# Kernel tuning notes

Measured on AMD Instinct MI355X. Metric: run time of the kernel, lower is better.

Reference implementation:

```python
import jax, jax.numpy as jnp
import numpy as np

N = 50000
E = 800000
GENE = 256
H = 128
BN_EPS = 1e-5


def _lin(key, fan_in, fan_out):
    k1, k2 = jax.random.split(key)
    w = jax.random.normal(k1, (fan_in, fan_out), jnp.float32) * (1.0 / np.sqrt(fan_in))
    b = jax.random.normal(k2, (fan_out,), jnp.float32) * 0.01
    return w, b


def setup_inputs() -> dict:
    key = jax.random.key(0)
    ks = jax.random.split(key, 32)
    inp = {}
    inp['x'] = jax.random.normal(ks[0], (N, GENE), jnp.float32)
    inp['edge_index'] = jax.random.randint(ks[1], (2, E), 0, N, jnp.int32)
    dims = [(GENE, H), (H, 2 * H), (2 * H, H), (H, H // 2)]
    ki = 2
    for i, (din, dout) in enumerate(dims, start=1):
        wa, ba = _lin(ks[ki], din, dout); ki += 1
        wb, bb = _lin(ks[ki], dout, dout); ki += 1
        inp[f'w{i}a'], inp[f'b{i}a'] = wa, ba
        inp[f'w{i}b'], inp[f'b{i}b'] = wb, bb
        inp[f'bn{i}_g'] = jnp.ones((dout,), jnp.float32)
        inp[f'bn{i}_b'] = jnp.zeros((dout,), jnp.float32)
        inp[f'bn{i}_m'] = jax.random.normal(ks[ki], (dout,), jnp.float32) * 0.1; ki += 1
        inp[f'bn{i}_v'] = jax.random.uniform(ks[ki], (dout,), jnp.float32, 0.5, 1.5); ki += 1
    wc, bc = _lin(ks[ki], H // 2, 2)
    inp['wc'], inp['bc'] = wc, bc
    return inp


def _gin_layer(h, src, dst, wa, ba, wb, bb, g, be, m, v):
    # GINConv (eps=0): z = x + sum_{j in N(i)} x_j, then 2-layer MLP
    agg = jax.ops.segment_sum(h[src], dst, num_segments=N)
    z = h + agg
    z = jax.nn.relu(z @ wa + ba) @ wb + bb
    # BatchNorm1d (eval: running stats) + ReLU
    z = (z - m) * jax.lax.rsqrt(v + BN_EPS) * g + be
    return jax.nn.relu(z)


def reference(x, edge_index,
              w1a, b1a, w1b, b1b, bn1_g, bn1_b, bn1_m, bn1_v,
              w2a, b2a, w2b, b2b, bn2_g, bn2_b, bn2_m, bn2_v,
              w3a, b3a, w3b, b3b, bn3_g, bn3_b, bn3_m, bn3_v,
              w4a, b4a, w4b, b4b, bn4_g, bn4_b, bn4_m, bn4_v,
              wc, bc):
    src, dst = edge_index[0], edge_index[1]
    h = _gin_layer(x, src, dst, w1a, b1a, w1b, b1b, bn1_g, bn1_b, bn1_m, bn1_v)
    h = _gin_layer(h, src, dst, w2a, b2a, w2b, b2b, bn2_g, bn2_b, bn2_m, bn2_v)
    h = _gin_layer(h, src, dst, w3a, b3a, w3b, b3b, bn3_g, bn3_b, bn3_m, bn3_v)
    h = _gin_layer(h, src, dst, w4a, b4a, w4b, b4b, bn4_g, bn4_b, bn4_m, bn4_v)
    return h @ wc + bc
```

## Files before the change

kernel.cpp:

```cpp
#include <hip/hip_runtime.h>

#define N_NODES 50000
#define N_EDGES 800000
#define BN_EPS 1e-5f
#define K_BUCK 196
#define PART_B 256
#define CHUNK 3125

typedef __attribute__((ext_vector_type(8))) short bshort8;
typedef __attribute__((ext_vector_type(4))) float f32x4;

__device__ inline float bf2f(unsigned int u16) {
    return __uint_as_float(u16 << 16);
}
__device__ inline unsigned short f2bf(float f) {
    unsigned int u = __float_as_uint(f);
    u = (u + 0x7FFFu + ((u >> 16) & 1u)) >> 16;
    return (unsigned short)u;
}


__device__ inline int block_exscan256(int v, int tid, int* total) {
    int lane = tid & 63;
    int wave = tid >> 6;
    int incl = v;
#pragma unroll
    for (int off = 1; off < 64; off <<= 1) {
        int t = __shfl_up(incl, off, 64);
        if (lane >= off) incl += t;
    }
    __shared__ int wsum[4];
    if (lane == 63) wsum[wave] = incl;
    __syncthreads();
    int w0 = wsum[0], w1 = wsum[1], w2 = wsum[2], w3 = wsum[3];
    __syncthreads();
    int wofs = (wave > 0 ? w0 : 0) + (wave > 1 ? w1 : 0) + (wave > 2 ? w2 : 0);
    *total = w0 + w1 + w2 + w3;
    return wofs + incl - v;
}

__global__ __launch_bounds__(256) void scan_reduce_kernel(const int* __restrict__ in,
                                                          int* __restrict__ bsum, int n) {
    int tid = threadIdx.x;
    int i = blockIdx.x * 256 + tid;
    int v = (i < n) ? in[i] : 0;
    int lane = tid & 63;
    int wave = tid >> 6;
#pragma unroll
    for (int off = 32; off > 0; off >>= 1) v += __shfl_down(v, off, 64);
    __shared__ int wsum[4];
    if (lane == 0) wsum[wave] = v;
    __syncthreads();
    if (tid == 0) bsum[blockIdx.x] = wsum[0] + wsum[1] + wsum[2] + wsum[3];
}

__global__ __launch_bounds__(256) void scan_bsum_kernel(int* __restrict__ bsum, int B) {
    int tid = threadIdx.x;
    int v = (tid < B) ? bsum[tid] : 0;
    int total;
    int excl = block_exscan256(v, tid, &total);
    if (tid < B) bsum[tid] = excl;
}

__global__ __launch_bounds__(256) void scan_apply_kernel(const int* __restrict__ in,
                                                         const int* __restrict__ bsum,
                                                         int* __restrict__ out, int n) {
    int tid = threadIdx.x;
    int i = blockIdx.x * 256 + tid;
    int v = (i < n) ? in[i] : 0;
    int total;
    int excl = block_exscan256(v, tid, &total);
    if (i < n) out[i] = bsum[blockIdx.x] + excl;
}


__global__ __launch_bounds__(256) void bucket_count_kernel(const int* __restrict__ dst,
                                                           int* __restrict__ deg,
                                                           int* __restrict__ cnt) {
    __shared__ int lcnt[K_BUCK];
    int tid = threadIdx.x;
    for (int i = tid; i < K_BUCK; i += 256) lcnt[i] = 0;
    __syncthreads();
    int start = blockIdx.x * CHUNK;
    for (int it = tid; it < CHUNK; it += 256) {
        int d = dst[start + it];
        atomicAdd(&lcnt[d >> 8], 1);
        atomicAdd(&deg[d], 1);
    }
    __syncthreads();
    for (int i = tid; i < K_BUCK; i += 256) cnt[i * PART_B + blockIdx.x] = lcnt[i];
}

__global__ __launch_bounds__(256) void partition_kernel(const int* __restrict__ src,
                                                        const int* __restrict__ dst,
                                                        const int* __restrict__ base,
                                                        uint2* __restrict__ P) {
    __shared__ int lofs[K_BUCK];
    int tid = threadIdx.x;
    for (int i = tid; i < K_BUCK; i += 256) lofs[i] = base[i * PART_B + blockIdx.x];
    __syncthreads();
    int start = blockIdx.x * CHUNK;
    for (int it = tid; it < CHUNK; it += 256) {
        int e = start + it;
        int d = dst[e], s = src[e];
        int p = atomicAdd(&lofs[d >> 8], 1);
        P[p] = make_uint2((unsigned)d, (unsigned)s);
    }
}

__global__ __launch_bounds__(256) void fine_scatter_kernel(const uint2* __restrict__ P,
                                                           const int* __restrict__ base,
                                                           const int* __restrict__ deg,
                                                           int* __restrict__ rowptr,
                                                           int* __restrict__ col) {
    __shared__ int wloc[256];
    int b = blockIdx.x;
    int tid = threadIdx.x;
    int nbase = b << 8;
    int nn = min(256, N_NODES - nbase);
    int d = (tid < nn) ? deg[nbase + tid] : 0;
    int total;
    int excl = block_exscan256(d, tid, &total);
    int start = base[b * PART_B];
    int rp = start + excl;
    if (tid < nn) {
        rowptr[nbase + tid] = rp;
        wloc[tid] = rp;
    }
    if (b == K_BUCK - 1 && tid == 0) rowptr[N_NODES] = N_EDGES;
    __syncthreads();
    int end = (b + 1 < K_BUCK) ? base[(b + 1) * PART_B] : N_EDGES;
    for (int e = start + tid; e < end; e += 256) {
        uint2 pr = P[e];
        int rank = atomicAdd(&wloc[pr.x - nbase], 1);
        col[rank] = (int)pr.y;
    }
}


struct WT8 {
    const float* src[8];
    unsigned short* dst[8];
    int K[8];
    int N[8];
};

__global__ __launch_bounds__(256) void wtconv_kernel(WT8 p) {
    int wi = blockIdx.y;
    int K = p.K[wi], N = p.N[wi];
    int idx = blockIdx.x * 256 + threadIdx.x;
    if (idx >= K * N) return;
    int logn = 31 - __clz(N);
    int n = idx & (N - 1);
    int k = idx >> logn;
    p.dst[wi][(size_t)n * K + k] = f2bf(p.src[wi][idx]);
}

__global__ __launch_bounds__(256) void wpconv_kernel(WT8 p) {
    int wi = blockIdx.y;
    int K = p.K[wi], N = p.N[wi];
    int idx = blockIdx.x * 256 + threadIdx.x;
    if (idx >= K * N) return;
    int S = K >> 5;
    int logs = 31 - __clz(S);
    int j = idx & 7;
    int l = (idx >> 3) & 63;
    int rest = idx >> 9;
    int s = rest & (S - 1);
    int t = rest >> logs;
    int k = s * 32 + ((l >> 4) << 3) + j;
    int n = t * 16 + (l & 15);
    p.dst[wi][idx] = f2bf(p.src[wi][(size_t)k * N + n]);
}


__device__ inline void acc8(uint4 v, float* a) {
    a[0] += bf2f(v.x & 0xFFFFu); a[1] += __uint_as_float(v.x & 0xFFFF0000u);
    a[2] += bf2f(v.y & 0xFFFFu); a[3] += __uint_as_float(v.y & 0xFFFF0000u);
    a[4] += bf2f(v.z & 0xFFFFu); a[5] += __uint_as_float(v.z & 0xFFFF0000u);
    a[6] += bf2f(v.w & 0xFFFFu); a[7] += __uint_as_float(v.w & 0xFFFF0000u);
}

template <int LPN, bool RELU>
__global__ __launch_bounds__(256) void aggregate_bf16_kernel(
    const unsigned short* __restrict__ h, const int* __restrict__ rowptr,
    const int* __restrict__ col, const float* __restrict__ bias,
    unsigned short* __restrict__ z, int n) {
    const int gpb = 256 / LPN;
    int gid = threadIdx.x / LPN;
    int l = threadIdx.x % LPN;
    int node = blockIdx.x * gpb + gid;
    if (node >= n) return;
    const uint4* hv = (const uint4*)h;
    float a[8] = {};
    uint4 vs = hv[(size_t)node * LPN + l];
    int s = rowptr[node], epos = rowptr[node + 1];
    int e = s;
    for (; e + 4 <= epos; e += 4) {
        int j0 = col[e], j1 = col[e + 1], j2 = col[e + 2], j3 = col[e + 3];
        uint4 v0 = hv[(size_t)j0 * LPN + l];
        uint4 v1 = hv[(size_t)j1 * LPN + l];
        uint4 v2 = hv[(size_t)j2 * LPN + l];
        uint4 v3 = hv[(size_t)j3 * LPN + l];
        acc8(v0, a); acc8(v1, a); acc8(v2, a); acc8(v3, a);
    }
    if (e + 1 < epos) {
        int j0 = col[e], j1 = col[e + 1];
        uint4 v0 = hv[(size_t)j0 * LPN + l];
        uint4 v1 = hv[(size_t)j1 * LPN + l];
        acc8(v0, a); acc8(v1, a);
        e += 2;
    }
    if (e < epos) {
        acc8(hv[(size_t)col[e] * LPN + l], a);
    }
    acc8(vs, a);
    if (RELU) {
        float4 b0 = *(const float4*)(bias + l * 8);
        float4 b1 = *(const float4*)(bias + l * 8 + 4);
        a[0] = fmaxf(a[0] + b0.x, 0.f); a[1] = fmaxf(a[1] + b0.y, 0.f);
        a[2] = fmaxf(a[2] + b0.z, 0.f); a[3] = fmaxf(a[3] + b0.w, 0.f);
        a[4] = fmaxf(a[4] + b1.x, 0.f); a[5] = fmaxf(a[5] + b1.y, 0.f);
        a[6] = fmaxf(a[6] + b1.z, 0.f); a[7] = fmaxf(a[7] + b1.w, 0.f);
    }
    uint4 o;
    o.x = (unsigned int)f2bf(a[0]) | ((unsigned int)f2bf(a[1]) << 16);
    o.y = (unsigned int)f2bf(a[2]) | ((unsigned int)f2bf(a[3]) << 16);
    o.z = (unsigned int)f2bf(a[4]) | ((unsigned int)f2bf(a[5]) << 16);
    o.w = (unsigned int)f2bf(a[6]) | ((unsigned int)f2bf(a[7]) << 16);
    ((uint4*)z)[(size_t)node * LPN + l] = o;
}


__device__ inline void epi_coeff(int mode, int c, const float* bias, const float* g,
                                 const float* be, const float* mu, const float* var,
                                 float* s, float* sh) {
    *s = 1.f; *sh = 0.f;
    if (mode == 0) {
        *sh = bias[c];
    } else if (mode == 1) {
        float t = g[c] * rsqrtf(var[c] + BN_EPS);
        *s = t;
        *sh = be[c] - mu[c] * t + bias[c] * t;
    }
}


template <int NT, bool F32A, bool CLS>
__global__ __launch_bounds__(256) void mfma_gemm2_kernel(
    const void* __restrict__ Ain, const unsigned short* __restrict__ Wt,
    const float* __restrict__ bias, unsigned short* __restrict__ C,
    int M, int K, int Nn, int mode, int gxblocks, int gy,
    const float* __restrict__ g, const float* __restrict__ be,
    const float* __restrict__ mu, const float* __restrict__ var,
    const float* __restrict__ wcls, const float* __restrict__ bcls,
    float* __restrict__ outp) {
    constexpr int BM = 128, BK = 64;
    constexpr int BN = NT * 16;
    constexpr int LDA = BK + 8;
    constexpr int LDB = BK + 8;
    constexpr int LDE = BN + 8;
    constexpr int NB_LD = (BN * BK / 8) / 256;
    __shared__ __align__(16) unsigned short smem[BM * LDA + BN * LDB];
    unsigned short* As = smem;
    unsigned short* Bs = smem + BM * LDA;
    unsigned short* Ep = smem;

    int id = blockIdx.x;
    int lo = id & 7;
    int t = id >> 3;
    int y = t % gy;
    int x = ((t / gy) << 3) | lo;
    if (x >= gxblocks) return;

    const int tid = threadIdx.x;
    const int wv = tid >> 6;
    const int ln = tid & 63;
    const int l15 = ln & 15;
    const int quad = ln >> 4;
    const int row0 = x * BM;
    const int col0 = y * BN;

    const unsigned short* A16 = (const unsigned short*)Ain;
    const float* A32 = (const float*)Ain;

    uint4 Ar[4], Br[NB_LD];

    auto loadA = [&](int k0) {
#pragma unroll
        for (int u = 0; u < 4; ++u) {
            int idx2 = tid + 256 * u;
            int r = idx2 >> 3, cg = (idx2 & 7) * 8;
            int gr = row0 + r;
            if (gr >= M) gr = M - 1;
            if (F32A) {
                float4 f0 = *(const float4*)(A32 + (size_t)gr * K + k0 + cg);
                float4 f1 = *(const float4*)(A32 + (size_t)gr * K + k0 + cg + 4);
                uint4 o;
                o.x = (unsigned)f2bf(f0.x) | ((unsigned)f2bf(f0.y) << 16);
                o.y = (unsigned)f2bf(f0.z) | ((unsigned)f2bf(f0.w) << 16);
                o.z = (unsigned)f2bf(f1.x) | ((unsigned)f2bf(f1.y) << 16);
                o.w = (unsigned)f2bf(f1.z) | ((unsigned)f2bf(f1.w) << 16);
                Ar[u] = o;
            } else {
                Ar[u] = *(const uint4*)(A16 + (size_t)gr * K + k0 + cg);
            }
        }
    };
    auto loadB = [&](int k0) {
#pragma unroll
        for (int u = 0; u < NB_LD; ++u) {
            int idx2 = tid + 256 * u;
            int r = idx2 >> 3, cg = (idx2 & 7) * 8;
            Br[u] = *(const uint4*)(Wt + (size_t)(col0 + r) * K + k0 + cg);
        }
    };
    auto stage = [&]() {
#pragma unroll
        for (int u = 0; u < 4; ++u) {
            int idx2 = tid + 256 * u;
            int r = idx2 >> 3, cg = (idx2 & 7) * 8;
            *(uint4*)(&As[r * LDA + cg]) = Ar[u];
        }
#pragma unroll
        for (int u = 0; u < NB_LD; ++u) {
            int idx2 = tid + 256 * u;
            int r = idx2 >> 3, cg = (idx2 & 7) * 8;
            *(uint4*)(&Bs[r * LDB + cg]) = Br[u];
        }
    };

    f32x4 acc[2][NT] = {};
    const int KT = K >> 6;
    loadA(0);
    loadB(0);
    for (int kt = 0; kt < KT; ++kt) {
        if (kt > 0) __syncthreads();
        stage();
        __syncthreads();
        if (kt + 1 < KT) {
            loadA((kt + 1) * 64);
            loadB((kt + 1) * 64);
        }
#pragma unroll
        for (int kh = 0; kh < 2; ++kh) {
            bshort8 af[2];
#pragma unroll
            for (int mt = 0; mt < 2; ++mt)
                af[mt] = *(const bshort8*)(&As[(wv * 32 + mt * 16 + l15) * LDA + kh * 32 + quad * 8]);
#pragma unroll
            for (int nt = 0; nt < NT; ++nt) {
                bshort8 bf = *(const bshort8*)(&Bs[(nt * 16 + l15) * LDB + kh * 32 + quad * 8]);
                acc[0][nt] = __builtin_amdgcn_mfma_f32_16x16x32_bf16(af[0], bf, acc[0][nt], 0, 0, 0);
                acc[1][nt] = __builtin_amdgcn_mfma_f32_16x16x32_bf16(af[1], bf, acc[1][nt], 0, 0, 0);
            }
        }
    }

    __syncthreads();
#pragma unroll
    for (int nt = 0; nt < NT; ++nt) {
        int c = col0 + nt * 16 + l15;
        float s, sh;
        epi_coeff(mode, c, bias, g, be, mu, var, &s, &sh);
#pragma unroll
        for (int mt = 0; mt < 2; ++mt) {
            int rl = wv * 32 + mt * 16 + quad * 4;
#pragma unroll
            for (int r = 0; r < 4; ++r) {
                float v = acc[mt][nt][r] * s + sh;
                if (mode != 2) v = fmaxf(v, 0.f);
                Ep[(rl + r) * LDE + nt * 16 + l15] = f2bf(v);
            }
        }
    }
    __syncthreads();
    if (CLS) {
        int r = tid >> 1, j = tid & 1;
        int grow = row0 + r;
        if (grow < M) {
            float s = 0.f;
#pragma unroll 8
            for (int k = 0; k < 64; ++k)
                s += bf2f(Ep[r * LDE + k]) * wcls[k * 2 + j];
            outp[(size_t)grow * 2 + j] = s + bcls[j];
        }
    } else {
        constexpr int CGR = BN / 8;
        constexpr int NU = BM * CGR / 256;
#pragma unroll
        for (int u = 0; u < NU; ++u) {
            int idx2 = tid + 256 * u;
            int r = idx2 / CGR, cg = (idx2 % CGR) * 8;
            int grow = row0 + r;
            if (grow < M)
                *(uint4*)(C + (size_t)grow * Nn + col0 + cg) = *(const uint4*)(&Ep[r * LDE + cg]);
        }
    }
}


template <int KIN, int DH>
__global__ __launch_bounds__(256, 4) void packed_gemm_kernel(
    const unsigned short* __restrict__ A, const unsigned short* __restrict__ Wp,
    int mode, const float* __restrict__ bias, const float* __restrict__ g,
    const float* __restrict__ be, const float* __restrict__ mu, const float* __restrict__ var,
    unsigned short* __restrict__ C, int M) {
    constexpr int BM = 64, BK = 64;
    constexpr int LDA = BK + 8;
    constexpr int LDE = DH + 8;
    constexpr int NT = DH / 64;
    constexpr int KT = KIN / 64;
    constexpr int S = KIN / 32;
    __shared__ __align__(16) unsigned short smem[BM * LDE];
    unsigned short* As = smem;
    unsigned short* Ep = smem;

    const int tid = threadIdx.x;
    const int wv = tid >> 6;
    const int ln = tid & 63;
    const int l15 = ln & 15;
    const int quad = ln >> 4;
    const int tb = wv * NT;
    const int ch = wv * (DH / 4);
    const int row0 = blockIdx.x * BM;

    uint4 Ar[2];
    auto loadA = [&](int k0) {
#pragma unroll
        for (int u = 0; u < 2; ++u) {
            int idx2 = tid + 256 * u;
            int r = idx2 >> 3, cg = (idx2 & 7) * 8;
            int gr = row0 + r;
            if (gr >= M) gr = M - 1;
            Ar[u] = *(const uint4*)(A + (size_t)gr * KIN + k0 + cg);
        }
    };
    auto stageA = [&]() {
#pragma unroll
        for (int u = 0; u < 2; ++u) {
            int idx2 = tid + 256 * u;
            int r = idx2 >> 3, cg = (idx2 & 7) * 8;
            *(uint4*)(&As[r * LDA + cg]) = Ar[u];
        }
    };
    auto loadB = [&](int s, bshort8* d) {
#pragma unroll
        for (int nt = 0; nt < NT; ++nt)
            d[nt] = *(const bshort8*)(Wp + ((size_t)((tb + nt) * S + s) * 64 + ln) * 8);
    };

    f32x4 acc[4][NT] = {};
    bshort8 bf[NT], bnx[NT];
    loadA(0);
    loadB(0, bf);
    for (int kt = 0; kt < KT; ++kt) {
        if (kt > 0) __syncthreads();
        stageA();
        __syncthreads();
        if (kt + 1 < KT) loadA((kt + 1) * 64);
#pragma unroll
        for (int kh = 0; kh < 2; ++kh) {
            int st = kt * 2 + kh;
            if (st + 1 < S) loadB(st + 1, bnx);
            bshort8 af[4];
#pragma unroll
            for (int mt = 0; mt < 4; ++mt)
                af[mt] = *(const bshort8*)(&As[(mt * 16 + l15) * LDA + kh * 32 + quad * 8]);
#pragma unroll
            for (int nt = 0; nt < NT; ++nt)
#pragma unroll
                for (int mt = 0; mt < 4; ++mt)
                    acc[mt][nt] = __builtin_amdgcn_mfma_f32_16x16x32_bf16(af[mt], bf[nt], acc[mt][nt], 0, 0, 0);
            if (st + 1 < S) {
#pragma unroll
                for (int nt = 0; nt < NT; ++nt) bf[nt] = bnx[nt];
            }
        }
    }
    __syncthreads();
#pragma unroll
    for (int nt = 0; nt < NT; ++nt) {
        int c = ch + nt * 16 + l15;
        float s, sh;
        epi_coeff(mode, c, bias, g, be, mu, var, &s, &sh);
#pragma unroll
        for (int mt = 0; mt < 4; ++mt) {
            int rl = mt * 16 + quad * 4;
#pragma unroll
            for (int r = 0; r < 4; ++r) {
                float v = acc[mt][nt][r] * s + sh;
                if (mode != 2) v = fmaxf(v, 0.f);
                Ep[(rl + r) * LDE + c] = f2bf(v);
            }
        }
    }
    __syncthreads();
    constexpr int CGR = DH / 8;
    constexpr int NU = BM * CGR / 256;
#pragma unroll
    for (int u = 0; u < NU; ++u) {
        int idx2 = tid + 256 * u;
        int r = idx2 / CGR, cg = (idx2 % CGR) * 8;
        int grow = row0 + r;
        if (grow < M)
            *(uint4*)(C + (size_t)grow * DH + cg) = *(const uint4*)(&Ep[r * LDE + cg]);
    }
}


template <int KIN, int DH1, int DH2>
__global__ __launch_bounds__(256, 3) void fused_mlp_kernel(
    const unsigned short* __restrict__ A,
    const unsigned short* __restrict__ Wp1, const unsigned short* __restrict__ Wp2,
    int mode1, const float* __restrict__ b1, const float* __restrict__ g1,
    const float* __restrict__ be1, const float* __restrict__ mu1, const float* __restrict__ var1,
    int mode2, const float* __restrict__ b2, const float* __restrict__ g2,
    const float* __restrict__ be2, const float* __restrict__ mu2, const float* __restrict__ var2,
    unsigned short* __restrict__ C, int M) {
    constexpr int BM = 64, BK = 64;
    constexpr int LDA = BK + 8;
    constexpr int LT1 = DH1 + 8;
    constexpr int LDE = DH2 + 8;
    constexpr int NT1 = DH1 / 64;
    constexpr int NT2 = DH2 / 64;
    constexpr int KT = KIN / 64;
    constexpr int S1 = KIN / 32;
    constexpr int S2 = DH1 / 32;
    __shared__ __align__(16) unsigned short smem[BM * LT1];
    unsigned short* As = smem;
    unsigned short* T1 = smem;

    const int tid = threadIdx.x;
    const int wv = tid >> 6;
    const int ln = tid & 63;
    const int l15 = ln & 15;
    const int quad = ln >> 4;
    const int tb1 = wv * NT1;
    const int tb2 = wv * NT2;
    const int ch1 = wv * (DH1 / 4);
    const int ch2 = wv * (DH2 / 4);
    const int row0 = blockIdx.x * BM;

    uint4 Ar[2];
    auto loadA = [&](int k0) {
#pragma unroll
        for (int u = 0; u < 2; ++u) {
            int idx2 = tid + 256 * u;
            int r = idx2 >> 3, cg = (idx2 & 7) * 8;
            int gr = row0 + r;
            if (gr >= M) gr = M - 1;
            Ar[u] = *(const uint4*)(A + (size_t)gr * KIN + k0 + cg);
        }
    };
    auto stageA = [&]() {
#pragma unroll
        for (int u = 0; u < 2; ++u) {
            int idx2 = tid + 256 * u;
            int r = idx2 >> 3, cg = (idx2 & 7) * 8;
            *(uint4*)(&As[r * LDA + cg]) = Ar[u];
        }
    };
    auto loadB1 = [&](int s, bshort8* d) {
#pragma unroll
        for (int nt = 0; nt < NT1; ++nt)
            d[nt] = *(const bshort8*)(Wp1 + ((size_t)((tb1 + nt) * S1 + s) * 64 + ln) * 8);
    };
    auto loadB2 = [&](int s, bshort8* d) {
#pragma unroll
        for (int nt = 0; nt < NT2; ++nt)
            d[nt] = *(const bshort8*)(Wp2 + ((size_t)((tb2 + nt) * S2 + s) * 64 + ln) * 8);
    };

    f32x4 acc1[4][NT1] = {};
    bshort8 bf[NT1], bnx[NT1], bf2[NT2];
    loadA(0);
    loadB1(0, bf);
    loadB2(0, bf2);
    for (int kt = 0; kt < KT; ++kt) {
        if (kt > 0) __syncthreads();
        stageA();
        __syncthreads();
        if (kt + 1 < KT) loadA((kt + 1) * 64);
#pragma unroll
        for (int kh = 0; kh < 2; ++kh) {
            int st = kt * 2 + kh;
            if (st + 1 < S1) loadB1(st + 1, bnx);
            bshort8 af[4];
#pragma unroll
            for (int mt = 0; mt < 4; ++mt)
                af[mt] = *(const bshort8*)(&As[(mt * 16 + l15) * LDA + kh * 32 + quad * 8]);
#pragma unroll
            for (int nt = 0; nt < NT1; ++nt)
#pragma unroll
                for (int mt = 0; mt < 4; ++mt)
                    acc1[mt][nt] = __builtin_amdgcn_mfma_f32_16x16x32_bf16(af[mt], bf[nt], acc1[mt][nt], 0, 0, 0);
            if (st + 1 < S1) {
#pragma unroll
                for (int nt = 0; nt < NT1; ++nt) bf[nt] = bnx[nt];
            }
        }
    }
    __syncthreads();
#pragma unroll
    for (int nt = 0; nt < NT1; ++nt) {
        int c = ch1 + nt * 16 + l15;
        float s, sh;
        epi_coeff(mode1, c, b1, g1, be1, mu1, var1, &s, &sh);
#pragma unroll
        for (int mt = 0; mt < 4; ++mt) {
            int rl = mt * 16 + quad * 4;
#pragma unroll
            for (int r = 0; r < 4; ++r) {
                float v = acc1[mt][nt][r] * s + sh;
                if (mode1 != 2) v = fmaxf(v, 0.f);
                T1[(rl + r) * LT1 + c] = f2bf(v);
            }
        }
    }
    __syncthreads();

    f32x4 acc2[4][NT2] = {};
    bshort8 bnx2[NT2];
#pragma unroll
    for (int ks = 0; ks < S2; ++ks) {
        if (ks + 1 < S2) loadB2(ks + 1, bnx2);
        bshort8 af[4];
#pragma unroll
        for (int mt = 0; mt < 4; ++mt)
            af[mt] = *(const bshort8*)(&T1[(mt * 16 + l15) * LT1 + ks * 32 + quad * 8]);
#pragma unroll
        for (int nt = 0; nt < NT2; ++nt)
#pragma unroll
            for (int mt = 0; mt < 4; ++mt)
                acc2[mt][nt] = __builtin_amdgcn_mfma_f32_16x16x32_bf16(af[mt], bf2[nt], acc2[mt][nt], 0, 0, 0);
        if (ks + 1 < S2) {
#pragma unroll
            for (int nt = 0; nt < NT2; ++nt) bf2[nt] = bnx2[nt];
        }
    }
    __syncthreads();

    unsigned short* Ep = T1;
#pragma unroll
    for (int nt = 0; nt < NT2; ++nt) {
        int c = ch2 + nt * 16 + l15;
        float s, sh;
        epi_coeff(mode2, c, b2, g2, be2, mu2, var2, &s, &sh);
#pragma unroll
        for (int mt = 0; mt < 4; ++mt) {
            int rl = mt * 16 + quad * 4;
#pragma unroll
            for (int r = 0; r < 4; ++r) {
                float v = acc2[mt][nt][r] * s + sh;
                if (mode2 != 2) v = fmaxf(v, 0.f);
                Ep[(rl + r) * LDE + c] = f2bf(v);
            }
        }
    }
    __syncthreads();
    constexpr int CGR = DH2 / 8;
    constexpr int NU = BM * CGR / 256;
#pragma unroll
    for (int u = 0; u < NU; ++u) {
        int idx2 = tid + 256 * u;
        int r = idx2 / CGR, cg = (idx2 % CGR) * 8;
        int grow = row0 + r;
        if (grow < M)
            *(uint4*)(C + (size_t)grow * DH2 + cg) = *(const uint4*)(&Ep[r * LDE + cg]);
    }
}


extern "C" void kernel_launch(void* const* d_in, const int* in_sizes, int n_in,
                              void* d_out, int out_size, void* d_ws, size_t ws_size,
                              hipStream_t stream) {
    const float* x = (const float*)d_in[0];
    const int* ei = (const int*)d_in[1];
    const int* src = ei;
    const int* dst = ei + N_EDGES;
    const float* w[4][2];
    const float* b[4][2];
    const float* bng[4];
    const float* bnb[4];
    const float* bnm[4];
    const float* bnv[4];
    int idx = 2;
    for (int i = 0; i < 4; ++i) {
        w[i][0] = (const float*)d_in[idx++];
        b[i][0] = (const float*)d_in[idx++];
        w[i][1] = (const float*)d_in[idx++];
        b[i][1] = (const float*)d_in[idx++];
        bng[i] = (const float*)d_in[idx++];
        bnb[i] = (const float*)d_in[idx++];
        bnm[i] = (const float*)d_in[idx++];
        bnv[i] = (const float*)d_in[idx++];
    }
    const float* wc = (const float*)d_in[idx++];
    const float* bc = (const float*)d_in[idx++];
    float* out = (float*)d_out;

    char* ws = (char*)d_ws;
    size_t off = 0;
    auto alloc = [&](size_t bytes) {
        char* p = ws + off;
        off = (off + bytes + 255) & ~(size_t)255;
        return p;
    };
    int* deg = (int*)alloc((size_t)N_NODES * 4);
    int* rowptr = (int*)alloc((size_t)(N_NODES + 1) * 4);
    int* cnt = (int*)alloc((size_t)K_BUCK * PART_B * 4);
    int* bsum2 = (int*)alloc((size_t)K_BUCK * 4);
    int* col = (int*)alloc((size_t)N_EDGES * 4);
    uint2* P = (uint2*)alloc((size_t)N_EDGES * 8);
    unsigned short* bufA = (unsigned short*)alloc((size_t)N_NODES * 256 * 2);
    unsigned short* bufB = (unsigned short*)alloc((size_t)N_NODES * 256 * 2);
    unsigned short* bufC = (unsigned short*)alloc((size_t)N_NODES * 256 * 2);
    const int dims_in[4] = {256, 128, 256, 128};
    const int dims_h[4] = {128, 256, 128, 64};
    unsigned short* wt[4][2];
    unsigned short* wp[4][2];
    for (int L = 0; L < 4; ++L) {
        wt[L][0] = (unsigned short*)alloc((size_t)dims_in[L] * dims_h[L] * 2);
        wt[L][1] = (unsigned short*)alloc((size_t)dims_h[L] * dims_h[L] * 2);
        wp[L][0] = (unsigned short*)alloc((size_t)dims_in[L] * dims_h[L] * 2);
        wp[L][1] = (unsigned short*)alloc((size_t)dims_h[L] * dims_h[L] * 2);
    }
    (void)ws_size;

    WT8 p;
    for (int L = 0; L < 4; ++L) {
        p.src[L * 2] = w[L][0];     p.dst[L * 2] = wt[L][0];
        p.K[L * 2] = dims_in[L];    p.N[L * 2] = dims_h[L];
        p.src[L * 2 + 1] = w[L][1]; p.dst[L * 2 + 1] = wt[L][1];
        p.K[L * 2 + 1] = dims_h[L]; p.N[L * 2 + 1] = dims_h[L];
    }
    wtconv_kernel<<<dim3(256, 8), 256, 0, stream>>>(p);
    WT8 q = p;
    for (int L = 0; L < 4; ++L) {
        q.dst[L * 2] = wp[L][0];
        q.dst[L * 2 + 1] = wp[L][1];
    }
    wpconv_kernel<<<dim3(256, 8), 256, 0, stream>>>(q);

    hipMemsetAsync(deg, 0, (size_t)N_NODES * 4, stream);
    bucket_count_kernel<<<PART_B, 256, 0, stream>>>(dst, deg, cnt);
    scan_reduce_kernel<<<K_BUCK, 256, 0, stream>>>(cnt, bsum2, K_BUCK * PART_B);
    scan_bsum_kernel<<<1, 256, 0, stream>>>(bsum2, K_BUCK);
    scan_apply_kernel<<<K_BUCK, 256, 0, stream>>>(cnt, bsum2, cnt, K_BUCK * PART_B);
    partition_kernel<<<PART_B, 256, 0, stream>>>(src, dst, cnt, P);
    fine_scatter_kernel<<<K_BUCK, 256, 0, stream>>>(P, cnt, deg, rowptr, col);

    const int gx = (N_NODES + 127) / 128;
    const int gxp = ((gx + 7) / 8) * 8;
    const int gx64 = (N_NODES + 63) / 64;
    const int M = N_NODES;

    mfma_gemm2_kernel<8, true, false><<<gxp, 256, 0, stream>>>(
        x, wt[0][0], nullptr, bufA, M, 256, 128, 2, gx, 1,
        nullptr, nullptr, nullptr, nullptr, nullptr, nullptr, nullptr);
    aggregate_bf16_kernel<16, true><<<(N_NODES + 15) / 16, 256, 0, stream>>>(
        bufA, rowptr, col, b[0][0], bufB, N_NODES);
    packed_gemm_kernel<128, 128><<<gx64, 256, 0, stream>>>(
        bufB, wp[0][1], 1, b[0][1], bng[0], bnb[0], bnm[0], bnv[0], bufC, M);

    aggregate_bf16_kernel<16, false><<<(N_NODES + 15) / 16, 256, 0, stream>>>(
        bufC, rowptr, col, nullptr, bufA, N_NODES);
    fused_mlp_kernel<128, 256, 256><<<gx64, 256, 0, stream>>>(
        bufA, wp[1][0], wp[1][1],
        0, b[1][0], nullptr, nullptr, nullptr, nullptr,
        1, b[1][1], bng[1], bnb[1], bnm[1], bnv[1],
        bufC, M);

    packed_gemm_kernel<256, 128><<<gx64, 256, 0, stream>>>(
        bufC, wp[2][0], 2, nullptr, nullptr, nullptr, nullptr, nullptr, bufA, M);
    aggregate_bf16_kernel<16, true><<<(N_NODES + 15) / 16, 256, 0, stream>>>(
        bufA, rowptr, col, b[2][0], bufB, N_NODES);

    fused_mlp_kernel<128, 128, 64><<<gx64, 256, 0, stream>>>(
        bufB, wp[2][1], wp[3][0],
        1, b[2][1], bng[2], bnb[2], bnm[2], bnv[2],
        2, nullptr, nullptr, nullptr, nullptr, nullptr,
        bufA, M);

    aggregate_bf16_kernel<8, true><<<(N_NODES + 31) / 32, 256, 0, stream>>>(
        bufA, rowptr, col, b[3][0], bufB, N_NODES);
    mfma_gemm2_kernel<4, false, true><<<gxp, 256, 0, stream>>>(
        bufB, wt[3][1], b[3][1], nullptr, M, 64, 64, 1, gx, 1,
        bng[3], bnb[3], bnm[3], bnv[3], wc, bc, out);
}
```

Before: 419.6 us.

## Fuse neighbor aggregation into following GEMM/MLP kernels via shared-memory head

```diff
diff --git a/kernel.cpp b/kernel.cpp
--- a/kernel.cpp
+++ b/kernel.cpp
@@ -181,54 +181,62 @@
     a[6] += bf2f(v.w & 0xFFFFu); a[7] += __uint_as_float(v.w & 0xFFFF0000u);
 }
 
-template <int LPN, bool RELU>
-__global__ __launch_bounds__(256) void aggregate_bf16_kernel(
-    const unsigned short* __restrict__ h, const int* __restrict__ rowptr,
-    const int* __restrict__ col, const float* __restrict__ bias,
-    unsigned short* __restrict__ z, int n) {
-    const int gpb = 256 / LPN;
-    int gid = threadIdx.x / LPN;
-    int l = threadIdx.x % LPN;
-    int node = blockIdx.x * gpb + gid;
-    if (node >= n) return;
+template <int KIN, bool RELU>
+__device__ inline void agg_head(const unsigned short* __restrict__ h,
+                                const int* __restrict__ rowptr,
+                                const int* __restrict__ col,
+                                const float* __restrict__ bias,
+                                unsigned short* __restrict__ As,
+                                int row0, int M, int tid) {
+    constexpr int LPN = KIN / 8;
+    constexpr int GPS = 256 / LPN;
+    constexpr int NSW = 64 / GPS;
+    constexpr int LDA = KIN + 8;
     const uint4* hv = (const uint4*)h;
-    float a[8] = {};
-    uint4 vs = hv[(size_t)node * LPN + l];
-    int s = rowptr[node], epos = rowptr[node + 1];
-    int e = s;
-    for (; e + 4 <= epos; e += 4) {
-        int j0 = col[e], j1 = col[e + 1], j2 = col[e + 2], j3 = col[e + 3];
-        uint4 v0 = hv[(size_t)j0 * LPN + l];
-        uint4 v1 = hv[(size_t)j1 * LPN + l];
-        uint4 v2 = hv[(size_t)j2 * LPN + l];
-        uint4 v3 = hv[(size_t)j3 * LPN + l];
-        acc8(v0, a); acc8(v1, a); acc8(v2, a); acc8(v3, a);
-    }
-    if (e + 1 < epos) {
-        int j0 = col[e], j1 = col[e + 1];
-        uint4 v0 = hv[(size_t)j0 * LPN + l];
-        uint4 v1 = hv[(size_t)j1 * LPN + l];
-        acc8(v0, a); acc8(v1, a);
-        e += 2;
-    }
-    if (e < epos) {
-        acc8(hv[(size_t)col[e] * LPN + l], a);
-    }
-    acc8(vs, a);
-    if (RELU) {
-        float4 b0 = *(const float4*)(bias + l * 8);
-        float4 b1 = *(const float4*)(bias + l * 8 + 4);
-        a[0] = fmaxf(a[0] + b0.x, 0.f); a[1] = fmaxf(a[1] + b0.y, 0.f);
-        a[2] = fmaxf(a[2] + b0.z, 0.f); a[3] = fmaxf(a[3] + b0.w, 0.f);
-        a[4] = fmaxf(a[4] + b1.x, 0.f); a[5] = fmaxf(a[5] + b1.y, 0.f);
-        a[6] = fmaxf(a[6] + b1.z, 0.f); a[7] = fmaxf(a[7] + b1.w, 0.f);
-    }
-    uint4 o;
-    o.x = (unsigned int)f2bf(a[0]) | ((unsigned int)f2bf(a[1]) << 16);
-    o.y = (unsigned int)f2bf(a[2]) | ((unsigned int)f2bf(a[3]) << 16);
-    o.z = (unsigned int)f2bf(a[4]) | ((unsigned int)f2bf(a[5]) << 16);
-    o.w = (unsigned int)f2bf(a[6]) | ((unsigned int)f2bf(a[7]) << 16);
-    ((uint4*)z)[(size_t)node * LPN + l] = o;
+    const int l = tid & (LPN - 1);
+    const int g = tid / LPN;
+#pragma unroll
+    for (int sw = 0; sw < NSW; ++sw) {
+        int r = sw * GPS + g;
+        int node = row0 + r;
+        uint4 o = make_uint4(0u, 0u, 0u, 0u);
+        if (node < M) {
+            float a[8] = {};
+            uint4 vs = hv[(size_t)node * LPN + l];
+            int s = rowptr[node], epos = rowptr[node + 1];
+            int e = s;
+            for (; e + 4 <= epos; e += 4) {
+                int j0 = col[e], j1 = col[e + 1], j2 = col[e + 2], j3 = col[e + 3];
+                uint4 v0 = hv[(size_t)j0 * LPN + l];
+                uint4 v1 = hv[(size_t)j1 * LPN + l];
+                uint4 v2 = hv[(size_t)j2 * LPN + l];
+                uint4 v3 = hv[(size_t)j3 * LPN + l];
+                acc8(v0, a); acc8(v1, a); acc8(v2, a); acc8(v3, a);
+            }
+            if (e + 1 < epos) {
+                int j0 = col[e], j1 = col[e + 1];
+                uint4 v0 = hv[(size_t)j0 * LPN + l];
+                uint4 v1 = hv[(size_t)j1 * LPN + l];
+                acc8(v0, a); acc8(v1, a);
+                e += 2;
+            }
+            if (e < epos) acc8(hv[(size_t)col[e] * LPN + l], a);
+            acc8(vs, a);
+            if (RELU) {
+                float4 b0 = *(const float4*)(bias + l * 8);
+                float4 b1 = *(const float4*)(bias + l * 8 + 4);
+                a[0] = fmaxf(a[0] + b0.x, 0.f); a[1] = fmaxf(a[1] + b0.y, 0.f);
+                a[2] = fmaxf(a[2] + b0.z, 0.f); a[3] = fmaxf(a[3] + b0.w, 0.f);
+                a[4] = fmaxf(a[4] + b1.x, 0.f); a[5] = fmaxf(a[5] + b1.y, 0.f);
+                a[6] = fmaxf(a[6] + b1.z, 0.f); a[7] = fmaxf(a[7] + b1.w, 0.f);
+            }
+            o.x = (unsigned int)f2bf(a[0]) | ((unsigned int)f2bf(a[1]) << 16);
+            o.y = (unsigned int)f2bf(a[2]) | ((unsigned int)f2bf(a[3]) << 16);
+            o.z = (unsigned int)f2bf(a[4]) | ((unsigned int)f2bf(a[5]) << 16);
+            o.w = (unsigned int)f2bf(a[6]) | ((unsigned int)f2bf(a[7]) << 16);
+        }
+        *(uint4*)(&As[r * LDA + l * 8]) = o;
+    }
 }
 
 
@@ -246,15 +254,11 @@
 }
 
 
-template <int NT, bool F32A, bool CLS>
+template <int NT, bool F32A>
 __global__ __launch_bounds__(256) void mfma_gemm2_kernel(
     const void* __restrict__ Ain, const unsigned short* __restrict__ Wt,
-    const float* __restrict__ bias, unsigned short* __restrict__ C,
-    int M, int K, int Nn, int mode, int gxblocks, int gy,
-    const float* __restrict__ g, const float* __restrict__ be,
-    const float* __restrict__ mu, const float* __restrict__ var,
-    const float* __restrict__ wcls, const float* __restrict__ bcls,
-    float* __restrict__ outp) {
+    unsigned short* __restrict__ C,
+    int M, int K, int Nn, int mode, int gxblocks, int gy) {
     constexpr int BM = 128, BK = 64;
     constexpr int BN = NT * 16;
     constexpr int LDA = BK + 8;
@@ -360,42 +364,27 @@
     __syncthreads();
 #pragma unroll
     for (int nt = 0; nt < NT; ++nt) {
-        int c = col0 + nt * 16 + l15;
-        float s, sh;
-        epi_coeff(mode, c, bias, g, be, mu, var, &s, &sh);
 #pragma unroll
         for (int mt = 0; mt < 2; ++mt) {
             int rl = wv * 32 + mt * 16 + quad * 4;
 #pragma unroll
             for (int r = 0; r < 4; ++r) {
-                float v = acc[mt][nt][r] * s + sh;
+                float v = acc[mt][nt][r];
                 if (mode != 2) v = fmaxf(v, 0.f);
                 Ep[(rl + r) * LDE + nt * 16 + l15] = f2bf(v);
             }
         }
     }
     __syncthreads();
-    if (CLS) {
-        int r = tid >> 1, j = tid & 1;
+    constexpr int CGR = BN / 8;
+    constexpr int NU = BM * CGR / 256;
+#pragma unroll
+    for (int u = 0; u < NU; ++u) {
+        int idx2 = tid + 256 * u;
+        int r = idx2 / CGR, cg = (idx2 % CGR) * 8;
         int grow = row0 + r;
-        if (grow < M) {
-            float s = 0.f;
-#pragma unroll 8
-            for (int k = 0; k < 64; ++k)
-                s += bf2f(Ep[r * LDE + k]) * wcls[k * 2 + j];
-            outp[(size_t)grow * 2 + j] = s + bcls[j];
-        }
-    } else {
-        constexpr int CGR = BN / 8;
-        constexpr int NU = BM * CGR / 256;
-#pragma unroll
-        for (int u = 0; u < NU; ++u) {
-            int idx2 = tid + 256 * u;
-            int r = idx2 / CGR, cg = (idx2 % CGR) * 8;
-            int grow = row0 + r;
-            if (grow < M)
-                *(uint4*)(C + (size_t)grow * Nn + col0 + cg) = *(const uint4*)(&Ep[r * LDE + cg]);
-        }
+        if (grow < M)
+            *(uint4*)(C + (size_t)grow * Nn + col0 + cg) = *(const uint4*)(&Ep[r * LDE + cg]);
     }
 }
 
@@ -509,25 +498,114 @@
 }
 
 
-template <int KIN, int DH1, int DH2>
-__global__ __launch_bounds__(256, 3) void fused_mlp_kernel(
-    const unsigned short* __restrict__ A,
+template <int KIN, int DH, bool ARELU>
+__global__ __launch_bounds__(256, 4) void agg_gemm_kernel(
+    const unsigned short* __restrict__ h, const int* __restrict__ rowptr,
+    const int* __restrict__ col, const float* __restrict__ abias,
+    const unsigned short* __restrict__ Wp,
+    int mode, const float* __restrict__ bias, const float* __restrict__ g,
+    const float* __restrict__ be, const float* __restrict__ mu, const float* __restrict__ var,
+    unsigned short* __restrict__ C, int M) {
+    constexpr int BM = 64;
+    constexpr int LDA = KIN + 8;
+    constexpr int LDE = DH + 8;
+    constexpr int NT = DH / 64;
+    constexpr int S = KIN / 32;
+    constexpr int LMX = (LDA > LDE) ? LDA : LDE;
+    __shared__ __align__(16) unsigned short smem[BM * LMX];
+    unsigned short* As = smem;
+    unsigned short* Ep = smem;
+
+    const int tid = threadIdx.x;
+    const int wv = tid >> 6;
+    const int ln = tid & 63;
+    const int l15 = ln & 15;
+    const int quad = ln >> 4;
+    const int tb = wv * NT;
+    const int ch = wv * (DH / 4);
+    const int row0 = blockIdx.x * BM;
+
+    auto loadB = [&](int s, bshort8* d) {
+#pragma unroll
+        for (int nt = 0; nt < NT; ++nt)
+            d[nt] = *(const bshort8*)(Wp + ((size_t)((tb + nt) * S + s) * 64 + ln) * 8);
+    };
+
+    bshort8 bf[NT], bnx[NT];
+    loadB(0, bf);
+    agg_head<KIN, ARELU>(h, rowptr, col, abias, As, row0, M, tid);
+    __syncthreads();
+
+    f32x4 acc[4][NT] = {};
+#pragma unroll
+    for (int ks = 0; ks < S; ++ks) {
+        if (ks + 1 < S) loadB(ks + 1, bnx);
+        bshort8 af[4];
+#pragma unroll
+        for (int mt = 0; mt < 4; ++mt)
+            af[mt] = *(const bshort8*)(&As[(mt * 16 + l15) * LDA + (ks >> 1) * 64 + (ks & 1) * 32 + quad * 8]);
+#pragma unroll
+        for (int nt = 0; nt < NT; ++nt)
+#pragma unroll
+            for (int mt = 0; mt < 4; ++mt)
+                acc[mt][nt] = __builtin_amdgcn_mfma_f32_16x16x32_bf16(af[mt], bf[nt], acc[mt][nt], 0, 0, 0);
+        if (ks + 1 < S) {
+#pragma unroll
+            for (int nt = 0; nt < NT; ++nt) bf[nt] = bnx[nt];
+        }
+    }
+    __syncthreads();
+#pragma unroll
+    for (int nt = 0; nt < NT; ++nt) {
+        int c = ch + nt * 16 + l15;
+        float s, sh;
+        epi_coeff(mode, c, bias, g, be, mu, var, &s, &sh);
+#pragma unroll
+        for (int mt = 0; mt < 4; ++mt) {
+            int rl = mt * 16 + quad * 4;
+#pragma unroll
+            for (int r = 0; r < 4; ++r) {
+                float v = acc[mt][nt][r] * s + sh;
+                if (mode != 2) v = fmaxf(v, 0.f);
+                Ep[(rl + r) * LDE + c] = f2bf(v);
+            }
+        }
+    }
+    __syncthreads();
+    constexpr int CGR = DH / 8;
+    constexpr int NU = BM * CGR / 256;
+#pragma unroll
+    for (int u = 0; u < NU; ++u) {
+        int idx2 = tid + 256 * u;
+        int r = idx2 / CGR, cg = (idx2 % CGR) * 8;
+        int grow = row0 + r;
+        if (grow < M)
+            *(uint4*)(C + (size_t)grow * DH + cg) = *(const uint4*)(&Ep[r * LDE + cg]);
+    }
+}
+
+
+template <int KIN, int DH1, int DH2, bool ARELU>
+__global__ __launch_bounds__(256, 3) void agg_mlp_kernel(
+    const unsigned short* __restrict__ h, const int* __restrict__ rowptr,
+    const int* __restrict__ col, const float* __restrict__ abias,
     const unsigned short* __restrict__ Wp1, const unsigned short* __restrict__ Wp2,
     int mode1, const float* __restrict__ b1, const float* __restrict__ g1,
     const float* __restrict__ be1, const float* __restrict__ mu1, const float* __restrict__ var1,
     int mode2, const float* __restrict__ b2, const float* __restrict__ g2,
     const float* __restrict__ be2, const float* __restrict__ mu2, const float* __restrict__ var2,
     unsigned short* __restrict__ C, int M) {
-    constexpr int BM = 64, BK = 64;
-    constexpr int LDA = BK + 8;
+    constexpr int BM = 64;
+    constexpr int LDA = KIN + 8;
     constexpr int LT1 = DH1 + 8;
     constexpr int LDE = DH2 + 8;
     constexpr int NT1 = DH1 / 64;
     constexpr int NT2 = DH2 / 64;
-    constexpr int KT = KIN / 64;
     constexpr int S1 = KIN / 32;
     constexpr int S2 = DH1 / 32;
-    __shared__ __align__(16) unsigned short smem[BM * LT1];
+    constexpr int LM0 = (LDA > LT1) ? LDA : LT1;
+    constexpr int LMX = (LM0 > LDE) ? LM0 : LDE;
+    __shared__ __align__(16) unsigned short smem[BM * LMX];
     unsigned short* As = smem;
     unsigned short* T1 = smem;
 
@@ -542,25 +620,6 @@
     const int ch2 = wv * (DH2 / 4);
     const int row0 = blockIdx.x * BM;
 
-    uint4 Ar[2];
-    auto loadA = [&](int k0) {
-#pragma unroll
-        for (int u = 0; u < 2; ++u) {
-            int idx2 = tid + 256 * u;
-            int r = idx2 >> 3, cg = (idx2 & 7) * 8;
-            int gr = row0 + r;
-            if (gr >= M) gr = M - 1;
-            Ar[u] = *(const uint4*)(A + (size_t)gr * KIN + k0 + cg);
-        }
-    };
-    auto stageA = [&]() {
-#pragma unroll
-        for (int u = 0; u < 2; ++u) {
-            int idx2 = tid + 256 * u;
-            int r = idx2 >> 3, cg = (idx2 & 7) * 8;
-            *(uint4*)(&As[r * LDA + cg]) = Ar[u];
-        }
-    };
     auto loadB1 = [&](int s, bshort8* d) {
 #pragma unroll
         for (int nt = 0; nt < NT1; ++nt)
@@ -572,33 +631,28 @@
             d[nt] = *(const bshort8*)(Wp2 + ((size_t)((tb2 + nt) * S2 + s) * 64 + ln) * 8);
     };
 
-    f32x4 acc1[4][NT1] = {};
     bshort8 bf[NT1], bnx[NT1], bf2[NT2];
-    loadA(0);
     loadB1(0, bf);
     loadB2(0, bf2);
-    for (int kt = 0; kt < KT; ++kt) {
-        if (kt > 0) __syncthreads();
-        stageA();
-        __syncthreads();
-        if (kt + 1 < KT) loadA((kt + 1) * 64);
-#pragma unroll
-        for (int kh = 0; kh < 2; ++kh) {
-            int st = kt * 2 + kh;
-            if (st + 1 < S1) loadB1(st + 1, bnx);
-            bshort8 af[4];
+    agg_head<KIN, ARELU>(h, rowptr, col, abias, As, row0, M, tid);
+    __syncthreads();
+
+    f32x4 acc1[4][NT1] = {};
+#pragma unroll
+    for (int ks = 0; ks < S1; ++ks) {
+        if (ks + 1 < S1) loadB1(ks + 1, bnx);
+        bshort8 af[4];
+#pragma unroll
+        for (int mt = 0; mt < 4; ++mt)
+            af[mt] = *(const bshort8*)(&As[(mt * 16 + l15) * LDA + (ks >> 1) * 64 + (ks & 1) * 32 + quad * 8]);
+#pragma unroll
+        for (int nt = 0; nt < NT1; ++nt)
 #pragma unroll
             for (int mt = 0; mt < 4; ++mt)
-                af[mt] = *(const bshort8*)(&As[(mt * 16 + l15) * LDA + kh * 32 + quad * 8]);
-#pragma unroll
-            for (int nt = 0; nt < NT1; ++nt)
-#pragma unroll
-                for (int mt = 0; mt < 4; ++mt)
-                    acc1[mt][nt] = __builtin_amdgcn_mfma_f32_16x16x32_bf16(af[mt], bf[nt], acc1[mt][nt], 0, 0, 0);
-            if (st + 1 < S1) {
-#pragma unroll
-                for (int nt = 0; nt < NT1; ++nt) bf[nt] = bnx[nt];
-            }
+                acc1[mt][nt] = __builtin_amdgcn_mfma_f32_16x16x32_bf16(af[mt], bf[nt], acc1[mt][nt], 0, 0, 0);
+        if (ks + 1 < S1) {
+#pragma unroll
+            for (int nt = 0; nt < NT1; ++nt) bf[nt] = bnx[nt];
         }
     }
     __syncthreads();
@@ -668,6 +722,84 @@
         int grow = row0 + r;
         if (grow < M)
             *(uint4*)(C + (size_t)grow * DH2 + cg) = *(const uint4*)(&Ep[r * LDE + cg]);
+    }
+}
+
+
+__global__ __launch_bounds__(256, 4) void agg_cls_kernel(
+    const unsigned short* __restrict__ h, const int* __restrict__ rowptr,
+    const int* __restrict__ col, const float* __restrict__ abias,
+    const unsigned short* __restrict__ Wp,
+    const float* __restrict__ bias, const float* __restrict__ g,
+    const float* __restrict__ be, const float* __restrict__ mu, const float* __restrict__ var,
+    const float* __restrict__ wcls, const float* __restrict__ bcls,
+    float* __restrict__ outp, int M) {
+    constexpr int BM = 64, KIN = 64, DH = 64;
+    constexpr int LDA = KIN + 8;
+    constexpr int LDE = DH + 8;
+    constexpr int NT = 1;
+    constexpr int S = KIN / 32;
+    __shared__ __align__(16) unsigned short smem[BM * LDA];
+    unsigned short* As = smem;
+    unsigned short* Ep = smem;
+
+    const int tid = threadIdx.x;
+    const int wv = tid >> 6;
+    const int ln = tid & 63;
+    const int l15 = ln & 15;
+    const int quad = ln >> 4;
+    const int tb = wv;
+    const int ch = wv * 16;
+    const int row0 = blockIdx.x * BM;
+
+    auto loadB = [&](int s, bshort8* d) {
+        d[0] = *(const bshort8*)(Wp + ((size_t)(tb * S + s) * 64 + ln) * 8);
+    };
+
+    bshort8 bf[NT], bnx[NT];
+    loadB(0, bf);
+    agg_head<KIN, true>(h, rowptr, col, abias, As, row0, M, tid);
+    __syncthreads();
+
+    f32x4 acc[4][NT] = {};
+#pragma unroll
+    for (int ks = 0; ks < S; ++ks) {
+        if (ks + 1 < S) loadB(ks + 1, bnx);
+        bshort8 af[4];
+#pragma unroll
+        for (int mt = 0; mt < 4; ++mt)
+            af[mt] = *(const bshort8*)(&As[(mt * 16 + l15) * LDA + ks * 32 + quad * 8]);
+#pragma unroll
+        for (int mt = 0; mt < 4; ++mt)
+            acc[mt][0] = __builtin_amdgcn_mfma_f32_16x16x32_bf16(af[mt], bf[0], acc[mt][0], 0, 0, 0);
+        if (ks + 1 < S) bf[0] = bnx[0];
+    }
+    __syncthreads();
+    {
+        int c = ch + l15;
+        float s, sh;
+        epi_coeff(1, c, bias, g, be, mu, var, &s, &sh);
+#pragma unroll
+        for (int mt = 0; mt < 4; ++mt) {
+            int rl = mt * 16 + quad * 4;
+#pragma unroll
+            for (int r = 0; r < 4; ++r) {
+                float v = fmaxf(acc[mt][0][r] * s + sh, 0.f);
+                Ep[(rl + r) * LDE + c] = f2bf(v);
+            }
+        }
+    }
+    __syncthreads();
+    if (tid < 128) {
+        int r = tid >> 1, j = tid & 1;
+        int grow = row0 + r;
+        if (grow < M) {
+            float s = 0.f;
+#pragma unroll 8
+            for (int k = 0; k < 64; ++k)
+                s += bf2f(Ep[r * LDE + k]) * wcls[k * 2 + j];
+            outp[(size_t)grow * 2 + j] = s + bcls[j];
+        }
     }
 }
 
@@ -756,36 +888,29 @@
     const int gx64 = (N_NODES + 63) / 64;
     const int M = N_NODES;
 
-    mfma_gemm2_kernel<8, true, false><<<gxp, 256, 0, stream>>>(
-        x, wt[0][0], nullptr, bufA, M, 256, 128, 2, gx, 1,
-        nullptr, nullptr, nullptr, nullptr, nullptr, nullptr, nullptr);
-    aggregate_bf16_kernel<16, true><<<(N_NODES + 15) / 16, 256, 0, stream>>>(
-        bufA, rowptr, col, b[0][0], bufB, N_NODES);
-    packed_gemm_kernel<128, 128><<<gx64, 256, 0, stream>>>(
-        bufB, wp[0][1], 1, b[0][1], bng[0], bnb[0], bnm[0], bnv[0], bufC, M);
-
-    aggregate_bf16_kernel<16, false><<<(N_NODES + 15) / 16, 256, 0, stream>>>(
-        bufC, rowptr, col, nullptr, bufA, N_NODES);
-    fused_mlp_kernel<128, 256, 256><<<gx64, 256, 0, stream>>>(
-        bufA, wp[1][0], wp[1][1],
+    mfma_gemm2_kernel<8, true><<<gxp, 256, 0, stream>>>(
+        x, wt[0][0], bufA, M, 256, 128, 2, gx, 1);
+
+    agg_gemm_kernel<128, 128, true><<<gx64, 256, 0, stream>>>(
+        bufA, rowptr, col, b[0][0], wp[0][1],
+        1, b[0][1], bng[0], bnb[0], bnm[0], bnv[0], bufC, M);
+
+    agg_mlp_kernel<128, 256, 256, false><<<gx64, 256, 0, stream>>>(
+        bufC, rowptr, col, nullptr, wp[1][0], wp[1][1],
         0, b[1][0], nullptr, nullptr, nullptr, nullptr,
         1, b[1][1], bng[1], bnb[1], bnm[1], bnv[1],
-        bufC, M);
+        bufA, M);
 
     packed_gemm_kernel<256, 128><<<gx64, 256, 0, stream>>>(
-        bufC, wp[2][0], 2, nullptr, nullptr, nullptr, nullptr, nullptr, bufA, M);
-    aggregate_bf16_kernel<16, true><<<(N_NODES + 15) / 16, 256, 0, stream>>>(
-        bufA, rowptr, col, b[2][0], bufB, N_NODES);
-
-    fused_mlp_kernel<128, 128, 64><<<gx64, 256, 0, stream>>>(
-        bufB, wp[2][1], wp[3][0],
+        bufA, wp[2][0], 2, nullptr, nullptr, nullptr, nullptr, nullptr, bufB, M);
+
+    agg_mlp_kernel<128, 128, 64, true><<<gx64, 256, 0, stream>>>(
+        bufB, rowptr, col, b[2][0], wp[2][1], wp[3][0],
         1, b[2][1], bng[2], bnb[2], bnm[2], bnv[2],
         2, nullptr, nullptr, nullptr, nullptr, nullptr,
-        bufA, M);
-
-    aggregate_bf16_kernel<8, true><<<(N_NODES + 31) / 32, 256, 0, stream>>>(
-        bufA, rowptr, col, b[3][0], bufB, N_NODES);
-    mfma_gemm2_kernel<4, false, true><<<gxp, 256, 0, stream>>>(
-        bufB, wt[3][1], b[3][1], nullptr, M, 64, 64, 1, gx, 1,
-        bng[3], bnb[3], bnm[3], bnv[3], wc, bc, out);
-}
+        bufC, M);
+
+    agg_cls_kernel<<<gx64, 256, 0, stream>>>(
+        bufC, rowptr, col, b[3][0], wp[3][1],
+        b[3][1], bng[3], bnb[3], bnm[3], bnv[3], wc, bc, out, M);
+}
```

Measured after the change: 419.5 us. About the same (-0.0%).
